# Optimization experiments

Measured on AMD Instinct MI355X. Metric: run time of the kernel, lower is better.

The kernel has to match this reference:

```python
import jax, jax.numpy as jnp
import numpy as np

N_EMBED = 1024
N_HEAD = 16
HEAD_DIM = N_EMBED // N_HEAD
NEG_BIG = 1e10


def setup_inputs() -> dict:
    key = jax.random.key(0)
    k1, k2, k3 = jax.random.split(key, 3)
    B, S = 2, 2048
    x = jax.random.normal(k1, (B, S, N_EMBED), dtype=jnp.float32)
    W_attn = jax.random.normal(k2, (N_EMBED, 3 * N_EMBED), dtype=jnp.float32) * 0.02
    b_attn = jnp.zeros((3 * N_EMBED,), dtype=jnp.float32)
    W_proj = jax.random.normal(k3, (N_EMBED, N_EMBED), dtype=jnp.float32) * 0.02
    b_proj = jnp.zeros((N_EMBED,), dtype=jnp.float32)
    return {"x": x, "W_attn": W_attn, "b_attn": b_attn, "W_proj": W_proj, "b_proj": b_proj}


def _split_heads(t):
    # [B, S, E] -> [B, H, S, Dh]
    B, S, _ = t.shape
    return t.reshape(B, S, N_HEAD, HEAD_DIM).transpose(0, 2, 1, 3)


def reference(x, W_attn, b_attn, W_proj, b_proj):
    B, S, E = x.shape
    qkv = x @ W_attn + b_attn  # fused QKV projection (Conv1D)
    q, k, v = jnp.split(qkv, 3, axis=-1)
    q, k, v = _split_heads(q), _split_heads(k), _split_heads(v)
    present = jnp.stack((k, v))  # [2, B, H, S, Dh]

    # naive causal attention: full [B,H,S,S] score matrix
    scores = jnp.einsum('bhqd,bhkd->bhqk', q, k)
    scores = scores / jnp.sqrt(jnp.asarray(HEAD_DIM, dtype=scores.dtype))  # scale=True
    mask = jnp.tril(jnp.ones((S, S), dtype=scores.dtype))[None, None]
    scores = scores * mask - NEG_BIG * (1.0 - mask)
    attn = jax.nn.softmax(scores, axis=-1)
    out = jnp.einsum('bhqk,bhkd->bhqd', attn, v)

    # merge heads: [B,H,S,Dh] -> [B,S,E]
    out = out.transpose(0, 2, 1, 3).reshape(B, S, E)
    out = out @ W_proj + b_proj
    return (out, present)
```

## Files before the change

kernel.cpp:

```cpp
#include <hip/hip_runtime.h>

typedef unsigned short u16;
typedef __attribute__((ext_vector_type(8))) __bf16 bf16x8;
typedef __attribute__((ext_vector_type(8))) u16 u16x8;
typedef __attribute__((ext_vector_type(4))) float f32x4;

#define DEV __device__ __forceinline__

DEV u16 f2bf(float f) {
  union { float f; unsigned u; } x; x.f = f;
  unsigned u = x.u;
  u += 0x7fffu + ((u >> 16) & 1u);
  return (u16)(u >> 16);
}

DEV void gload16(const void* g, void* l) {
  __builtin_amdgcn_global_load_lds(
      (const __attribute__((address_space(1))) void*)g,
      (__attribute__((address_space(3))) void*)l, 16, 0, 0);
}

DEV f32x4 mfma16(bf16x8 a, bf16x8 b, f32x4 c) {
  return __builtin_amdgcn_mfma_f32_16x16x32_bf16(a, b, c, 0, 0, 0);
}

DEV void bar() {
  asm volatile("" ::: "memory");
  __builtin_amdgcn_s_barrier();
  asm volatile("" ::: "memory");
}

#define SEQ   2048
#define EMB   1024
#define MROWS 4096
#define NQKV  3072
#define HID   64
#define PRESENT_HALF 4194304
#define QSCALE 0.1803368801f

__global__ void k_convert(const float* __restrict__ src, u16* __restrict__ dst, int n8) {
  int i = blockIdx.x * blockDim.x + threadIdx.x;
  if (i >= n8) return;
  const float4* s = (const float4*)src + (size_t)i * 2;
  float4 a = s[0], b = s[1];
  u16x8 r;
  r[0] = f2bf(a.x); r[1] = f2bf(a.y); r[2] = f2bf(a.z); r[3] = f2bf(a.w);
  r[4] = f2bf(b.x); r[5] = f2bf(b.y); r[6] = f2bf(b.z); r[7] = f2bf(b.w);
  *((u16x8*)dst + i) = r;
}

__global__ void k_transpose(const float* __restrict__ src, u16* __restrict__ dst,
                            int K, int N) {
  __shared__ __attribute__((aligned(16))) u16 t[32][33];
  int n0 = blockIdx.x * 32, k0 = blockIdx.y * 32;
  for (int i = threadIdx.x; i < 1024; i += 256) {
    int r = i >> 5, c = i & 31;
    t[r][c] = f2bf(src[(size_t)(k0 + r) * N + (n0 + c)]);
  }
  __syncthreads();
  for (int i = threadIdx.x; i < 1024; i += 256) {
    int r = i >> 5, c = i & 31;
    dst[(size_t)(n0 + r) * K + (k0 + c)] = t[c][r];
  }
}

DEV void gemm_core(const u16* __restrict__ A, const u16* __restrict__ Bt, int K,
                   int brow, int bcol, u16* As, u16* Bs, f32x4 acc[4][4]) {
  int tid = threadIdx.x, lane = tid & 63, wid = tid >> 6;
  int wr = (wid >> 1) * 64, wc = (wid & 1) * 64;
  int r = lane & 15, kkb = (lane >> 4) * 16;
  const char* Ab = (const char*)(A + (size_t)(brow + (tid >> 2)) * K) + (tid & 3) * 16;
  const char* Bb = (const char*)(Bt + (size_t)(bcol + (tid >> 2)) * K) + (tid & 3) * 16;
  char* Ad = (char*)As + tid * 16;
  char* Bd = (char*)Bs + tid * 16;
  const size_t rowskip = (size_t)64 * K * 2;
  for (int k0 = 0; k0 < K; k0 += 32) {
    __syncthreads();
    size_t kb2 = (size_t)k0 * 2;
    gload16(Ab + kb2, Ad);
    gload16(Ab + kb2 + rowskip, Ad + 4096);
    gload16(Bb + kb2, Bd);
    gload16(Bb + kb2 + rowskip, Bd + 4096);
    __syncthreads();
    bf16x8 af[4], bfr[4];
#pragma unroll
    for (int m = 0; m < 4; ++m)
      af[m] = *(const bf16x8*)((const char*)As + (wr + m * 16 + r) * 64 + kkb);
#pragma unroll
    for (int n = 0; n < 4; ++n)
      bfr[n] = *(const bf16x8*)((const char*)Bs + (wc + n * 16 + r) * 64 + kkb);
#pragma unroll
    for (int m = 0; m < 4; ++m)
#pragma unroll
      for (int n = 0; n < 4; ++n)
        acc[m][n] = mfma16(af[m], bfr[n], acc[m][n]);
  }
}

DEV void xcd_swz(int nbx, int nby, int& bx, int& by) {
  int nwg = nbx * nby;
  int bid = by * nbx + bx;
  int cpx = nwg >> 3;
  int s = (bid & 7) * cpx + (bid >> 3);
  bx = s % nbx;
  by = s / nbx;
}

__global__ void k_gemm_qkv(const u16* __restrict__ A, const u16* __restrict__ Bt,
                           const float* __restrict__ bias, u16* __restrict__ qb,
                           u16* __restrict__ kb, u16* __restrict__ vt,
                           float* __restrict__ present) {
  __shared__ __attribute__((aligned(16))) u16 As[128 * 32];
  __shared__ __attribute__((aligned(16))) u16 Bs[128 * 32];
  f32x4 acc[4][4];
#pragma unroll
  for (int m = 0; m < 4; ++m)
#pragma unroll
    for (int n = 0; n < 4; ++n) acc[m][n] = {0.f, 0.f, 0.f, 0.f};
  int bx = blockIdx.x, by = blockIdx.y;
  xcd_swz(24, 32, bx, by);
  int brow = by * 128, bcol = bx * 128;
  gemm_core(A, Bt, EMB, brow, bcol, As, Bs, acc);
  int tid = threadIdx.x, lane = tid & 63, wid = tid >> 6;
  int wr = (wid >> 1) * 64, wc = (wid & 1) * 64;
  int r = lane & 15, rj = (lane >> 4) * 4;
#pragma unroll
  for (int m = 0; m < 4; ++m)
#pragma unroll
    for (int n = 0; n < 4; ++n) {
      int gc = bcol + wc + n * 16 + r;
      int t = gc >> 10, e = gc & 1023, h = e >> 6, dh = e & 63;
      float bv = bias[gc];
#pragma unroll
      for (int j = 0; j < 4; ++j) {
        int gr = brow + wr + m * 16 + rj + j;
        int bb = gr >> 11, s = gr & 2047;
        float v = acc[m][n][j] + bv;
        size_t hidx = (((size_t)(bb * 16 + h)) * SEQ + s) * HID + dh;
        if (t == 0)
          qb[hidx] = f2bf(v * QSCALE);
        else if (t == 1) {
          kb[hidx] = f2bf(v);
          present[hidx] = v;
        } else {
          vt[(((size_t)(bb * 16 + h)) * HID + dh) * SEQ + s] = f2bf(v);
          present[(size_t)PRESENT_HALF + hidx] = v;
        }
      }
    }
}

__global__ void k_gemm_proj(const u16* __restrict__ A, const u16* __restrict__ Bt,
                            const float* __restrict__ bias, float* __restrict__ out) {
  __shared__ __attribute__((aligned(16))) u16 As[128 * 32];
  __shared__ __attribute__((aligned(16))) u16 Bs[128 * 32];
  f32x4 acc[4][4];
#pragma unroll
  for (int m = 0; m < 4; ++m)
#pragma unroll
    for (int n = 0; n < 4; ++n) acc[m][n] = {0.f, 0.f, 0.f, 0.f};
  int bx = blockIdx.x, by = blockIdx.y;
  xcd_swz(8, 32, bx, by);
  int brow = by * 128, bcol = bx * 128;
  gemm_core(A, Bt, EMB, brow, bcol, As, Bs, acc);
  int tid = threadIdx.x, lane = tid & 63, wid = tid >> 6;
  int wr = (wid >> 1) * 64, wc = (wid & 1) * 64;
  int r = lane & 15, rj = (lane >> 4) * 4;
#pragma unroll
  for (int m = 0; m < 4; ++m)
#pragma unroll
    for (int n = 0; n < 4; ++n) {
      int gc = bcol + wc + n * 16 + r;
      float bv = bias[gc];
#pragma unroll
      for (int j = 0; j < 4; ++j) {
        int gr = brow + wr + m * 16 + rj + j;
        out[(size_t)gr * EMB + gc] = acc[m][n][j] + bv;
      }
    }
}

__global__ __launch_bounds__(256, 4) void k_attn(
    const u16* __restrict__ qb, const u16* __restrict__ kb,
    const u16* __restrict__ vt, u16* __restrict__ ao) {
  __shared__ __attribute__((aligned(16))) u16 Ks[2][4096];
  __shared__ __attribute__((aligned(16))) u16 Vs[2][4096];
  __shared__ __attribute__((aligned(16))) u16 Ps[4096];
  int tid = threadIdx.x, lane = tid & 63, w = tid >> 6;
  int r = lane & 15, g = lane >> 4, kkb = g * 16;
  int bid = blockIdx.x;
  int chunk = bid >> 8, tsub = (bid >> 5) & 7, bh = bid & 31;
  int t = (chunk == 0) ? (31 - tsub)
        : (chunk == 1) ? (16 + tsub)
        : (chunk == 2) ? (15 - tsub) : tsub;
  int q0 = t * 64;
  int ktmax = t;
  const char* Kbh = (const char*)kb + (size_t)bh * SEQ * 128;
  const char* Vbh = (const char*)vt + (size_t)bh * HID * SEQ * 2;

  size_t qr = (size_t)bh * SEQ + q0 + w * 16 + r;
  bf16x8 aq0 = *(const bf16x8*)((const char*)qb + qr * 128 + kkb);
  bf16x8 aq1 = *(const bf16x8*)((const char*)qb + qr * 128 + 64 + kkb);

  f32x4 o[4];
  float l[4];
#pragma unroll
  for (int d = 0; d < 4; ++d) o[d] = {0.f, 0.f, 0.f, 0.f};
#pragma unroll
  for (int j = 0; j < 4; ++j) l[j] = 0.f;

  int lin0 = tid * 16, lin1 = lin0 + 4096;
  int ks0 = lin0 ^ (((lin0 >> 7) & 7) << 4);
  int ks1 = lin1 ^ (((lin1 >> 7) & 7) << 4);
  int vr0 = lin0 >> 7, vc0 = (lin0 & 127) ^ ((vr0 & 7) << 4);
  int vr1 = lin1 >> 7, vc1 = (lin1 & 127) ^ ((vr1 & 7) << 4);

#define STAGE(kt, b) do {                                             \
    const char* Kg = Kbh + (size_t)(kt) * 8192;                       \
    gload16(Kg + ks0, (char*)Ks[b] + lin0);                           \
    gload16(Kg + ks1, (char*)Ks[b] + lin1);                           \
    const char* Vg = Vbh + (size_t)(kt) * 128;                        \
    gload16(Vg + (size_t)vr0 * 4096 + vc0, (char*)Vs[b] + lin0);      \
    gload16(Vg + (size_t)vr1 * 4096 + vc1, (char*)Vs[b] + lin1);      \
  } while (0)

  char* Pw = (char*)Ps + w * 2048;
  int swz = (r & 7) << 4;

  STAGE(0, 0);
  for (int kt = 0; kt <= ktmax; ++kt) {
    int cur = kt & 1;
    if (kt < ktmax) {
      STAGE(kt + 1, cur ^ 1);
      asm volatile("s_waitcnt vmcnt(4)" ::: "memory");
    } else {
      asm volatile("s_waitcnt vmcnt(0)" ::: "memory");
    }
    bar();
    const char* Kc = (const char*)Ks[cur];
    const char* Vc = (const char*)Vs[cur];

    f32x4 s[4];
    __builtin_amdgcn_s_setprio(1);
#pragma unroll
    for (int kc = 0; kc < 4; ++kc) {
      int rowb = (kc * 16 + r) * 128;
      bf16x8 bk0 = *(const bf16x8*)(Kc + ((rowb + kkb) ^ swz));
      bf16x8 bk1 = *(const bf16x8*)(Kc + ((rowb + 64 + kkb) ^ swz));
      f32x4 sv = {0.f, 0.f, 0.f, 0.f};
      sv = mfma16(aq0, bk0, sv);
      sv = mfma16(aq1, bk1, sv);
      s[kc] = sv;
    }
    __builtin_amdgcn_s_setprio(0);
    if (kt == ktmax) {
      int qg = q0 + w * 16 + g * 4;
#pragma unroll
      for (int kc = 0; kc < 4; ++kc) {
        int kg = kt * 64 + kc * 16 + r;
#pragma unroll
        for (int j = 0; j < 4; ++j)
          if (kg > qg + j) s[kc][j] = -1e30f;
      }
    }
#pragma unroll
    for (int kc = 0; kc < 4; ++kc)
#pragma unroll
      for (int j = 0; j < 4; ++j) {
        int row = g * 4 + j;
        int byt = (row * 128 + kc * 32 + r * 2) ^ ((row & 7) << 4);
        float p = __builtin_amdgcn_exp2f(s[kc][j]);
        l[j] += p;
        *(u16*)(Pw + byt) = f2bf(p);
      }
    __builtin_amdgcn_s_setprio(1);
#pragma unroll
    for (int kk2 = 0; kk2 < 2; ++kk2) {
      int pbyt = (r * 128 + kk2 * 64 + kkb) ^ swz;
      bf16x8 ap = *(const bf16x8*)(Pw + pbyt);
#pragma unroll
      for (int d = 0; d < 4; ++d) {
        int vrow = (d * 16 + r) * 128;
        bf16x8 bv = *(const bf16x8*)(Vc + ((vrow + kk2 * 64 + kkb) ^ swz));
        o[d] = mfma16(ap, bv, o[d]);
      }
    }
    __builtin_amdgcn_s_setprio(0);
    bar();
  }
#undef STAGE

  int b = bh >> 4, h = bh & 15;
#pragma unroll
  for (int j = 0; j < 4; ++j) {
    float sr = l[j];
    sr += __shfl_xor(sr, 1);
    sr += __shfl_xor(sr, 2);
    sr += __shfl_xor(sr, 4);
    sr += __shfl_xor(sr, 8);
    float inv = 1.f / sr;
    size_t row = (size_t)b * SEQ + q0 + w * 16 + g * 4 + j;
#pragma unroll
    for (int d = 0; d < 4; ++d)
      ao[row * EMB + h * 64 + d * 16 + r] = f2bf(o[d][j] * inv);
  }
}

extern "C" void kernel_launch(void* const* d_in, const int* in_sizes, int n_in,
                              void* d_out, int out_size, void* d_ws, size_t ws_size,
                              hipStream_t stream) {
  const float* x = (const float*)d_in[0];
  const float* W_attn = (const float*)d_in[1];
  const float* b_attn = (const float*)d_in[2];
  const float* W_proj = (const float*)d_in[3];
  const float* b_proj = (const float*)d_in[4];
  float* out = (float*)d_out;
  char* ws = (char*)d_ws;
  u16* xb  = (u16*)(ws + 0);
  u16* wat = (u16*)(ws + 8388608);
  u16* wpt = (u16*)(ws + 14680064);
  u16* qb  = (u16*)(ws + 16777216);
  u16* kb  = (u16*)(ws + 25165824);
  u16* vtb = (u16*)(ws + 33554432);
  u16* ao  = (u16*)(ws + 41943040);
  float* present = out + PRESENT_HALF;

  k_convert<<<dim3(2048), 256, 0, stream>>>(x, xb, 524288);
  k_transpose<<<dim3(96, 32), 256, 0, stream>>>(W_attn, wat, EMB, NQKV);
  k_transpose<<<dim3(32, 32), 256, 0, stream>>>(W_proj, wpt, EMB, EMB);
  k_gemm_qkv<<<dim3(24, 32), 256, 0, stream>>>(xb, wat, b_attn, qb, kb, vtb, present);
  k_attn<<<dim3(1024), 256, 0, stream>>>(qb, kb, vtb, ao);
  k_gemm_proj<<<dim3(8, 32), 256, 0, stream>>>(ao, wpt, b_proj, out);
}
```

Baseline: 121.3 us.

## Double-buffer LDS tiles in GEMM core to overlap global loads with MFMA

The shared GEMM core used by the QKV and projection kernels now keeps two LDS buffers per operand. It prefetches the next K-slice with global_load_lds while computing the current one, and uses explicit vmcnt waits and barriers in place of load-then-sync per iteration. The goal is to hide global memory latency behind MFMA work, at the cost of doubling shared memory per block, which may reduce occupancy. An extra lgkmcnt wait is also added before the barrier in the attention loop.

```diff
diff --git a/kernel.cpp b/kernel.cpp
--- a/kernel.cpp
+++ b/kernel.cpp
@@ -74,27 +74,40 @@
   char* Ad = (char*)As + tid * 16;
   char* Bd = (char*)Bs + tid * 16;
   const size_t rowskip = (size_t)64 * K * 2;
-  for (int k0 = 0; k0 < K; k0 += 32) {
-    __syncthreads();
-    size_t kb2 = (size_t)k0 * 2;
-    gload16(Ab + kb2, Ad);
-    gload16(Ab + kb2 + rowskip, Ad + 4096);
-    gload16(Bb + kb2, Bd);
-    gload16(Bb + kb2 + rowskip, Bd + 4096);
-    __syncthreads();
+#define GSTAGE(k0v, b) do { size_t kb2 = (size_t)(k0v) * 2;            \
+    gload16(Ab + kb2, Ad + (b) * 8192);                                \
+    gload16(Ab + kb2 + rowskip, Ad + (b) * 8192 + 4096);               \
+    gload16(Bb + kb2, Bd + (b) * 8192);                                \
+    gload16(Bb + kb2 + rowskip, Bd + (b) * 8192 + 4096); } while (0)
+  GSTAGE(0, 0);
+  int nk = K >> 5;
+  for (int i = 0; i < nk; ++i) {
+    int cur = i & 1;
+    if (i < nk - 1) {
+      GSTAGE((i + 1) << 5, cur ^ 1);
+      asm volatile("s_waitcnt vmcnt(4)" ::: "memory");
+    } else {
+      asm volatile("s_waitcnt vmcnt(0)" ::: "memory");
+    }
+    bar();
+    const char* Ac = (const char*)As + cur * 8192;
+    const char* Bc = (const char*)Bs + cur * 8192;
     bf16x8 af[4], bfr[4];
 #pragma unroll
     for (int m = 0; m < 4; ++m)
-      af[m] = *(const bf16x8*)((const char*)As + (wr + m * 16 + r) * 64 + kkb);
+      af[m] = *(const bf16x8*)(Ac + (wr + m * 16 + r) * 64 + kkb);
 #pragma unroll
     for (int n = 0; n < 4; ++n)
-      bfr[n] = *(const bf16x8*)((const char*)Bs + (wc + n * 16 + r) * 64 + kkb);
+      bfr[n] = *(const bf16x8*)(Bc + (wc + n * 16 + r) * 64 + kkb);
 #pragma unroll
     for (int m = 0; m < 4; ++m)
 #pragma unroll
       for (int n = 0; n < 4; ++n)
         acc[m][n] = mfma16(af[m], bfr[n], acc[m][n]);
-  }
+    asm volatile("s_waitcnt lgkmcnt(0)" ::: "memory");
+    bar();
+  }
+#undef GSTAGE
 }
 
 DEV void xcd_swz(int nbx, int nby, int& bx, int& by) {
@@ -110,8 +123,8 @@
                            const float* __restrict__ bias, u16* __restrict__ qb,
                            u16* __restrict__ kb, u16* __restrict__ vt,
                            float* __restrict__ present) {
-  __shared__ __attribute__((aligned(16))) u16 As[128 * 32];
-  __shared__ __attribute__((aligned(16))) u16 Bs[128 * 32];
+  __shared__ __attribute__((aligned(16))) u16 As[2 * 4096];
+  __shared__ __attribute__((aligned(16))) u16 Bs[2 * 4096];
   f32x4 acc[4][4];
 #pragma unroll
   for (int m = 0; m < 4; ++m)
@@ -152,8 +165,8 @@
 
 __global__ void k_gemm_proj(const u16* __restrict__ A, const u16* __restrict__ Bt,
                             const float* __restrict__ bias, float* __restrict__ out) {
-  __shared__ __attribute__((aligned(16))) u16 As[128 * 32];
-  __shared__ __attribute__((aligned(16))) u16 Bs[128 * 32];
+  __shared__ __attribute__((aligned(16))) u16 As[2 * 4096];
+  __shared__ __attribute__((aligned(16))) u16 Bs[2 * 4096];
   f32x4 acc[4][4];
 #pragma unroll
   for (int m = 0; m < 4; ++m)
@@ -286,6 +299,7 @@
       }
     }
     __builtin_amdgcn_s_setprio(0);
+    asm volatile("s_waitcnt lgkmcnt(0)" ::: "memory");
     bar();
   }
 #undef STAGE
```

Measured after the change: 122.5 us. Within noise of the previous version (+1.0%).
